# Optimization experiments

Measured on AMD Instinct MI355X. Metric: run time of the kernel, lower is better.

Reference implementation:

```python
import jax, jax.numpy as jnp
import numpy as np

N_RAYS, N_SAMPLES = 65536, 128


def setup_inputs() -> dict:
    key = jax.random.key(0)
    k1, k2, k3, k4, k5 = jax.random.split(key, 5)
    return {
        "sigma_vals": jax.random.normal(k1, (N_RAYS, N_SAMPLES), dtype=jnp.float32),
        "rgb_vals": jax.random.uniform(k2, (N_RAYS, N_SAMPLES, 3), dtype=jnp.float32),
        "dists": jax.random.uniform(k3, (N_RAYS, N_SAMPLES), dtype=jnp.float32),
        "z_vals": jax.random.uniform(k4, (N_RAYS, N_SAMPLES), dtype=jnp.float32),
        "bg_color": jax.random.uniform(k5, (N_RAYS, 3), dtype=jnp.float32),
    }


def composite(sigma_vals, dists):
    # tau = relu(sigma) * dist; alpha = 1 - exp(-tau)
    tau = jax.nn.relu(sigma_vals) * dists
    alpha = 1.0 - jnp.exp(-tau)                       # [N, S]
    # inclusive cumprod of (1 - alpha + eps), with leading ones -> transmittance [N, S+1]
    trans = jnp.cumprod(1.0 - alpha + 1e-10, axis=-1)
    transmittance = jnp.concatenate(
        [jnp.ones_like(alpha[..., :1]), trans], axis=-1
    )
    w = alpha * transmittance[..., :-1]               # [N, S]
    return w, transmittance


def reference(sigma_vals, rgb_vals, dists, z_vals, bg_color):
    # Python-side compositing path of Raymarcher.render_train (thresh=0).
    weights, transmittance = composite(sigma_vals, dists)
    no_hit = transmittance[..., -1]                                    # [N]
    color = (weights[..., None] * rgb_vals).sum(axis=-2)               # [N, 3]
    color = color + no_hit[..., None] * bg_color                       # bg compositing
    depth = (weights * z_vals).sum(axis=-1)                            # [N]
    # pack color+depth into one array so the output is a single tensor [N, 4]
    return jnp.concatenate([color, depth[:, None]], axis=-1)
```

## Files before the change

### kernel.cpp

```cpp
#include <hip/hip_runtime.h>


#define SAMPLES 128
#define LANES_PER_RAY 16

template <int CTRL>
__device__ __forceinline__ float fdpp(float oldv, float src) {
    return __uint_as_float((unsigned)__builtin_amdgcn_update_dpp(
        (int)__float_as_uint(oldv), (int)__float_as_uint(src),
        CTRL, 0xF, 0xF, false));
}

__global__ __launch_bounds__(256) void raymarch_composite(
    const float* __restrict__ sigma,
    const float* __restrict__ rgb,
    const float* __restrict__ dists,
    const float* __restrict__ zvals,
    const float* __restrict__ bg,
    float* __restrict__ out,
    int n_rays)
{
    const int lane = threadIdx.x & 63;
    const int gw   = blockIdx.x * (blockDim.x >> 6) + (threadIdx.x >> 6);
    const int grp  = lane >> 4;
    const int pos  = lane & 15;
    const int ray  = gw * 4 + grp;
    if (ray >= n_rays) return;

    const size_t sbase = (size_t)ray * SAMPLES + pos * 8;
    const float4* sp = reinterpret_cast<const float4*>(sigma + sbase);
    const float4* dp = reinterpret_cast<const float4*>(dists + sbase);
    const float4* zp = reinterpret_cast<const float4*>(zvals + sbase);
    const float4* cp = reinterpret_cast<const float4*>(
        rgb + (size_t)ray * (SAMPLES * 3) + pos * 24);

    const float4 s0 = sp[0], s1 = sp[1];
    const float4 d0 = dp[0], d1 = dp[1];
    const float4 z0 = zp[0], z1 = zp[1];
    const float4 c0 = cp[0], c1 = cp[1], c2 = cp[2];
    const float4 c3 = cp[3], c4 = cp[4], c5 = cp[5];
    const float bgv = (pos < 3) ? bg[(size_t)ray * 3 + pos] : 0.0f;

    const float s[8] = {s0.x, s0.y, s0.z, s0.w, s1.x, s1.y, s1.z, s1.w};
    const float d[8] = {d0.x, d0.y, d0.z, d0.w, d1.x, d1.y, d1.z, d1.w};
    const float z[8] = {z0.x, z0.y, z0.z, z0.w, z1.x, z1.y, z1.z, z1.w};
    const float c[24] = {c0.x, c0.y, c0.z, c0.w, c1.x, c1.y, c1.z, c1.w,
                         c2.x, c2.y, c2.z, c2.w, c3.x, c3.y, c3.z, c3.w,
                         c4.x, c4.y, c4.z, c4.w, c5.x, c5.y, c5.z, c5.w};

    const float eps = 1e-10f;
    float t = 1.0f;
    float r = 0.f, g = 0.f, b = 0.f, dep = 0.f;
    #pragma unroll
    for (int i = 0; i < 8; ++i) {
        const float tau = fmaxf(s[i], 0.0f) * d[i];
        const float e   = __expf(-tau);
        const float a   = 1.0f - e;
        const float f   = e + eps;
        const float w   = a * t;
        r   = fmaf(w, c[3 * i + 0], r);
        g   = fmaf(w, c[3 * i + 1], g);
        b   = fmaf(w, c[3 * i + 2], b);
        dep = fmaf(w, z[i], dep);
        t *= f;
    }

    float sc = t;
    sc *= fdpp<0x111>(1.0f, sc);
    sc *= fdpp<0x112>(1.0f, sc);
    sc *= fdpp<0x114>(1.0f, sc);
    sc *= fdpp<0x118>(1.0f, sc);
    const float excl = fdpp<0x111>(1.0f, sc);

    const float no_hit = __shfl(sc, lane | 15);

    r *= excl; g *= excl; b *= excl; dep *= excl;

    const bool o1 = pos & 1;
    float X  = o1 ? g : r, Xo = o1 ? r : g;
    float Y  = o1 ? dep : b, Yo = o1 ? b : dep;
    X += fdpp<0xB1>(0.0f, Xo);
    Y += fdpp<0xB1>(0.0f, Yo);
    const bool o2 = pos & 2;
    float Z  = o2 ? Y : X, Zo = o2 ? X : Y;
    Z += fdpp<0x4E>(0.0f, Zo);
    Z += fdpp<0x124>(0.0f, Z);
    Z += fdpp<0x128>(0.0f, Z);

    if (pos < 4) {
        out[(size_t)ray * 4 + pos] = fmaf(no_hit, bgv, Z);
    }
}

extern "C" void kernel_launch(void* const* d_in, const int* in_sizes, int n_in,
                              void* d_out, int out_size, void* d_ws, size_t ws_size,
                              hipStream_t stream) {
    const float* sigma = (const float*)d_in[0];
    const float* rgb   = (const float*)d_in[1];
    const float* dists = (const float*)d_in[2];
    const float* zvals = (const float*)d_in[3];
    const float* bg    = (const float*)d_in[4];
    float* out = (float*)d_out;

    const int n_rays = in_sizes[0] / SAMPLES;
    const int rays_per_block = 16;
    const int grid = (n_rays + rays_per_block - 1) / rays_per_block;

    raymarch_composite<<<grid, 256, 0, stream>>>(sigma, rgb, dists, zvals, bg,
                                                 out, n_rays);
}
```

Baseline: 217.0 us.

## Stage per-wave loads through LDS for fully coalesced global reads

Each wave now loads its four rays' sigma, dists, z and rgb data with lane-contiguous float4 reads, so every load instruction covers a contiguous 1 KB span. The data is then transposed through padded shared memory back into the per-lane 8-sample layout the scan needs. This targets the strided per-lane access pattern of the old direct loads, at the cost of LDS writes and reads, extra waitcnts, and more shared memory per block, which can lower occupancy. The reduction code is only reformatted.

```diff
diff --git a/kernel.cpp b/kernel.cpp
--- a/kernel.cpp
+++ b/kernel.cpp
@@ -2,7 +2,6 @@
 
 
 #define SAMPLES 128
-#define LANES_PER_RAY 16
 
 template <int CTRL>
 __device__ __forceinline__ float fdpp(float oldv, float src) {
@@ -10,6 +9,8 @@
         (int)__float_as_uint(oldv), (int)__float_as_uint(src),
         CTRL, 0xF, 0xF, false));
 }
+
+#define WAVE_GRANS 396
 
 __global__ __launch_bounds__(256) void raymarch_composite(
     const float* __restrict__ sigma,
@@ -20,30 +21,61 @@
     float* __restrict__ out,
     int n_rays)
 {
+    __shared__ float4 lds4[4 * WAVE_GRANS];
+
     const int lane = threadIdx.x & 63;
-    const int gw   = blockIdx.x * (blockDim.x >> 6) + (threadIdx.x >> 6);
+    const int wave = threadIdx.x >> 6;
+    const int gw   = blockIdx.x * 4 + wave;
     const int grp  = lane >> 4;
     const int pos  = lane & 15;
-    const int ray  = gw * 4 + grp;
-    if (ray >= n_rays) return;
+    const int ray0 = gw * 4;
+    const int ray  = ray0 + grp;
+    if (ray0 >= n_rays) return;
+    const int wb = wave * WAVE_GRANS;
 
-    const size_t sbase = (size_t)ray * SAMPLES + pos * 8;
-    const float4* sp = reinterpret_cast<const float4*>(sigma + sbase);
-    const float4* dp = reinterpret_cast<const float4*>(dists + sbase);
-    const float4* zp = reinterpret_cast<const float4*>(zvals + sbase);
-    const float4* cp = reinterpret_cast<const float4*>(
-        rgb + (size_t)ray * (SAMPLES * 3) + pos * 24);
+    const float4* sg = reinterpret_cast<const float4*>(sigma + (size_t)ray0 * SAMPLES);
+    const float4* dg = reinterpret_cast<const float4*>(dists + (size_t)ray0 * SAMPLES);
+    const float4* zg = reinterpret_cast<const float4*>(zvals + (size_t)ray0 * SAMPLES);
+    const float4* cg = reinterpret_cast<const float4*>(rgb   + (size_t)ray0 * SAMPLES * 3);
 
-    const float4 s0 = sp[0], s1 = sp[1];
-    const float4 d0 = dp[0], d1 = dp[1];
-    const float4 z0 = zp[0], z1 = zp[1];
-    const float4 c0 = cp[0], c1 = cp[1], c2 = cp[2];
-    const float4 c3 = cp[3], c4 = cp[4], c5 = cp[5];
+    const float4 sv0 = sg[lane],       sv1 = sg[lane + 64];
+    const float4 dv0 = dg[lane],       dv1 = dg[lane + 64];
+    const float4 zv0 = zg[lane],       zv1 = zg[lane + 64];
+    const float4 cv0 = cg[lane],       cv1 = cg[lane + 64],  cv2 = cg[lane + 128];
+    const float4 cv3 = cg[lane + 192], cv4 = cg[lane + 256], cv5 = cg[lane + 320];
     const float bgv = (pos < 3) ? bg[(size_t)ray * 3 + pos] : 0.0f;
 
-    const float s[8] = {s0.x, s0.y, s0.z, s0.w, s1.x, s1.y, s1.z, s1.w};
-    const float d[8] = {d0.x, d0.y, d0.z, d0.w, d1.x, d1.y, d1.z, d1.w};
-    const float z[8] = {z0.x, z0.y, z0.z, z0.w, z1.x, z1.y, z1.z, z1.w};
+    {
+        const int r0 = lane >> 5,        G0 = lane & 31;
+        const int r1 = (lane + 64) >> 5, G1 = lane & 31;
+        const int w0 = wb + r0 * 33 + G0, w1 = wb + r1 * 33 + G1;
+        lds4[w0 +   0] = sv0;  lds4[w1 +   0] = sv1;
+        lds4[w0 + 132] = dv0;  lds4[w1 + 132] = dv1;
+        lds4[w0 + 264] = zv0;  lds4[w1 + 264] = zv1;
+    }
+    asm volatile("s_waitcnt lgkmcnt(0)" ::: "memory");
+
+    const int abase = wb + grp * 33 + 2 * pos;
+    const float4 s01 = lds4[abase +   0], s23 = lds4[abase +   0 + 1];
+    const float4 d01 = lds4[abase + 132], d23 = lds4[abase + 132 + 1];
+    const float4 z01 = lds4[abase + 264], z23 = lds4[abase + 264 + 1];
+    asm volatile("s_waitcnt lgkmcnt(0)" ::: "memory");
+
+    lds4[wb + lane] = cv0;
+    lds4[wb + ((lane < 32) ? lane + 64 : lane + 65)] = cv1;
+    lds4[wb + lane + 129] = cv2;
+    lds4[wb + lane + 194] = cv3;
+    lds4[wb + ((lane < 32) ? lane + 258 : lane + 259)] = cv4;
+    lds4[wb + lane + 323] = cv5;
+    asm volatile("s_waitcnt lgkmcnt(0)" ::: "memory");
+
+    const int cbase = wb + grp * 97 + 6 * pos;
+    const float4 c0 = lds4[cbase + 0], c1 = lds4[cbase + 1], c2 = lds4[cbase + 2];
+    const float4 c3 = lds4[cbase + 3], c4 = lds4[cbase + 4], c5 = lds4[cbase + 5];
+
+    const float s[8] = {s01.x, s01.y, s01.z, s01.w, s23.x, s23.y, s23.z, s23.w};
+    const float d[8] = {d01.x, d01.y, d01.z, d01.w, d23.x, d23.y, d23.z, d23.w};
+    const float z[8] = {z01.x, z01.y, z01.z, z01.w, z23.x, z23.y, z23.z, z23.w};
     const float c[24] = {c0.x, c0.y, c0.z, c0.w, c1.x, c1.y, c1.z, c1.w,
                          c2.x, c2.y, c2.z, c2.w, c3.x, c3.y, c3.z, c3.w,
                          c4.x, c4.y, c4.z, c4.w, c5.x, c5.y, c5.z, c5.w};
@@ -77,13 +109,10 @@
     r *= excl; g *= excl; b *= excl; dep *= excl;
 
     const bool o1 = pos & 1;
-    float X  = o1 ? g : r, Xo = o1 ? r : g;
-    float Y  = o1 ? dep : b, Yo = o1 ? b : dep;
-    X += fdpp<0xB1>(0.0f, Xo);
-    Y += fdpp<0xB1>(0.0f, Yo);
+    float X = (o1 ? g : r) + fdpp<0xB1>(0.0f, o1 ? r : g);
+    float Y = (o1 ? dep : b) + fdpp<0xB1>(0.0f, o1 ? b : dep);
     const bool o2 = pos & 2;
-    float Z  = o2 ? Y : X, Zo = o2 ? X : Y;
-    Z += fdpp<0x4E>(0.0f, Zo);
+    float Z = (o2 ? Y : X) + fdpp<0x4E>(0.0f, o2 ? X : Y);
     Z += fdpp<0x124>(0.0f, Z);
     Z += fdpp<0x128>(0.0f, Z);
 
```

Result: no change. 216.3 us (-0.3%).
